# Performance work log

Hardware: AMD Instinct MI355X
Metric: run time of the kernel (lower is better)

## Reference

```python
import jax, jax.numpy as jnp
import numpy as np

EPS = 1e-6

def _exp_map0(v):
    # v: [..., D] tangent at origin with v[...,0]==0
    sp = v[..., 1:]
    n = jnp.sqrt(jnp.clip(jnp.sum(sp * sp, -1, keepdims=True), EPS))
    return jnp.concatenate([jnp.cosh(n), jnp.sinh(n) / n * sp], -1)

def _log_map0(x):
    x0 = x[..., :1]
    sp = x[..., 1:]
    n = jnp.sqrt(jnp.clip(jnp.sum(sp * sp, -1, keepdims=True), EPS))
    d = jnp.arccosh(jnp.clip(x0, 1.0 + EPS))
    return jnp.concatenate([jnp.zeros_like(x0), d / n * sp], -1)

def _pt_to_origin(x, v):
    # parallel transport v from T_x to T_o, o=(1,0,...,0):
    # PT(v) = v + <o,v>_L / (1 - <x,o>_L) * (x + o);  <o,v>_L=-v0, <x,o>_L=-x0
    coef = -v[..., :1] / (1.0 + x[..., :1])
    x_plus_o = jnp.concatenate([x[..., :1] + 1.0, x[..., 1:]], -1)
    return v + coef * x_plus_o

def _linear(h, W, b):
    # torch nn.Linear: h @ W.T + b, W: [out, in]
    return jnp.einsum('bne,de->bnd', h, W) + b

def setup_inputs() -> dict:
    key = jax.random.key(0)
    ks = jax.random.split(key, 8)
    B, N, d = 8, 2048, 256
    # manifold points via exp_map0 of small tangents
    t = jax.random.normal(ks[0], (B, N, d), jnp.float32) * 0.1
    x = _exp_map0(jnp.pad(t, ((0, 0), (0, 0), (1, 0))))
    # tangent velocity at x: project random u onto T_x (add <x,u>_L * x since <x,x>_L=-1)
    u = jax.random.normal(ks[1], (B, N, d + 1), jnp.float32) * 0.1
    xu = jnp.sum(x * u, -1, keepdims=True) - 2.0 * x[..., :1] * u[..., :1]  # Lorentz inner
    x_vel = u + xu * x
    s = 1.0 / np.sqrt(d)
    Wq = jax.random.normal(ks[2], (d, d), jnp.float32) * s
    Wk = jax.random.normal(ks[3], (d, d), jnp.float32) * s
    Wv = jax.random.normal(ks[4], (d, d), jnp.float32) * s
    bq = jnp.zeros((d,), jnp.float32)
    bk = jnp.zeros((d,), jnp.float32)
    bv = jnp.zeros((d,), jnp.float32)
    tau = jnp.ones((1,), jnp.float32)
    return {"x": x, "x_vel": x_vel, "Wq": Wq, "bq": bq, "Wk": Wk, "bk": bk,
            "Wv": Wv, "bv": bv, "tau": tau}

def reference(x, x_vel, Wq, bq, Wk, bk, Wv, bv, tau):
    lambda_penalty = 1.0
    log_x = _log_map0(x)
    x_tan = log_x[..., 1:]                                   # [B,N,d]
    q_s = _linear(x_tan, Wq, bq)
    k_s = _linear(x_tan, Wk, bk)
    v_s = _linear(x_tan, Wv, bv)
    pad = lambda h: jnp.pad(h, ((0, 0), (0, 0), (1, 0)))
    q = _exp_map0(pad(q_s))                                  # [B,N,D]
    k = _exp_map0(pad(k_s))
    log_v = pad(v_s)
    vel0 = _pt_to_origin(x, x_vel)
    q_vel = _linear(vel0[..., 1:], Wq, bq)                   # [B,N,d]
    k_vel = _linear(vel0[..., 1:], Wk, bk)
    # pairwise Lorentz distance: <q,k>_L = sum(q*k) - 2*q0*k0
    inner = jnp.einsum('bnd,bmd->bnm', q, k) \
            - 2.0 * q[..., 0][:, :, None] * k[..., 0][:, None, :]
    d_L = jnp.arccosh(jnp.clip(-inner, 1.0 + EPS))           # [B,N,N]
    q_sq = jnp.sum(q_vel * q_vel, -1)                        # [B,N]
    k_sq = jnp.sum(k_vel * k_vel, -1)
    qk = jnp.einsum('bnd,bmd->bnm', q_vel, k_vel)
    pen = jnp.clip(q_sq[:, :, None] + k_sq[:, None, :] - 2.0 * qk, 0.0)
    tau_c = jnp.clip(tau, 0.001)[0]
    logits = -(1.0 / tau_c) * d_L ** 2 - lambda_penalty * pen
    attn = jax.nn.softmax(logits, axis=-1)                   # [B,N,N]
    agg = jnp.einsum('bnm,bmd->bnd', attn, log_v)
    z = _exp_map0(agg)
    return z, attn, x_tan
```

## Files before the change

kernel.cpp:

```cpp
#include <hip/hip_runtime.h>
#include <math.h>

#define BB 8
#define NN 2048
#define DD 256
#define TT (BB*NN)
#define DP1 257
#define EPSF 1e-6f

typedef _Float16 f16;
typedef __attribute__((ext_vector_type(8))) _Float16 f16x8;
typedef __attribute__((ext_vector_type(4))) float f32x4;

#define BAR() asm volatile("s_barrier" ::: "memory")
#define WAIT_VM(N) asm volatile("s_waitcnt vmcnt(" #N ")" ::: "memory")
#define WAIT_LGKM0() asm volatile("s_waitcnt lgkmcnt(0)" ::: "memory")

__device__ __forceinline__ f32x4 mfma16(f16x8 a, f16x8 b, f32x4 c) {
  return __builtin_amdgcn_mfma_f32_16x16x32_f16(a, b, c, 0, 0, 0);
}
__device__ __forceinline__ void gll16(const f16* g, f16* l) {
  __builtin_amdgcn_global_load_lds(
      (const __attribute__((address_space(1))) void*)g,
      (__attribute__((address_space(3))) void*)l, 16, 0, 0);
}

__device__ __forceinline__ float wave_sum(float v) {
#pragma unroll
  for (int m = 1; m < 64; m <<= 1) v += __shfl_xor(v, m);
  return v;
}

__global__ __launch_bounds__(256) void prep_kernel(
    const float* __restrict__ x, const float* __restrict__ xv,
    float* __restrict__ xtan, f16* __restrict__ xtan_h, f16* __restrict__ vel0_h) {
  const int w = threadIdx.x >> 6, l = threadIdx.x & 63;
  const int tok = blockIdx.x * 4 + w;
  const float* xr = x  + (size_t)tok * DP1;
  const float* vr = xv + (size_t)tok * DP1;
  float x0 = xr[0];
  float sp[4];
  float ss = 0.f;
#pragma unroll
  for (int j = 0; j < 4; j++) { sp[j] = xr[1 + l + 64 * j]; ss = fmaf(sp[j], sp[j], ss); }
  ss = wave_sum(ss);
  float n  = sqrtf(fmaxf(ss, EPSF));
  float dd = acoshf(fmaxf(x0, 1.f + EPSF));
  float scl = dd / n;
  float coef = -vr[0] / (1.f + x0);
  const size_t base = (size_t)tok * DD;
#pragma unroll
  for (int j = 0; j < 4; j++) {
    float xt = scl * sp[j];
    xtan[base + l + 64 * j] = xt;
    xtan_h[base + l + 64 * j] = (f16)xt;
    vel0_h[base + l + 64 * j] = (f16)(vr[1 + l + 64 * j] + coef * sp[j]);
  }
}

__global__ __launch_bounds__(256) void wcast_kernel(
    const float* __restrict__ Wq, const float* __restrict__ Wk,
    const float* __restrict__ Wv, f16* __restrict__ Wh) {
  const int m = blockIdx.y;
  const int i = blockIdx.x * 256 + threadIdx.x;
  const float* W = (m == 0) ? Wq : ((m == 1) ? Wk : Wv);
  Wh[(size_t)m * DD * DD + i] = (f16)W[i];
}

__global__ __launch_bounds__(256, 2) void gemm_mfma(
    const f16* __restrict__ xtan_h, const f16* __restrict__ vel0_h,
    const f16* __restrict__ Wh,
    f16* __restrict__ qh, f16* __restrict__ kh, f16* __restrict__ vT,
    f16* __restrict__ qvh, f16* __restrict__ kvh,
    const float* __restrict__ bq, const float* __restrict__ bk,
    const float* __restrict__ bv) {
  __shared__ __align__(16) f16 sA[2 * 4096];
  __shared__ __align__(16) f16 sB[2 * 4096];
  const int tid = threadIdx.x;
  const int bm = blockIdx.x * 128;
  const int bn = blockIdx.y * 128;
  const int seg = bn >> 8;
  const int w = tid >> 6, l = tid & 63;
  const int wr = w >> 1, wc = w & 1;
  f32x4 acc[4][4] = {};
  const f16* Ab = ((seg < 3) ? xtan_h : vel0_h) + (size_t)bm * DD;
  const f16* Bb = Wh + (size_t)((seg < 3) ? bn : (bn - 768)) * DD;

  auto stage = [&](int nx) {
    const int half = nx & 1, k0 = nx * 32;
#pragma unroll
    for (int p = 0; p < 2; p++) {
      int u = tid + p * 256;
      int row = u >> 2;
      int q = (u & 3) ^ ((u >> 3) & 3);
      size_t go = (size_t)row * DD + k0 + q * 8;
      size_t lb = (size_t)half * 4096 + (size_t)(w * 64 + p * 256) * 8;
      gll16(Ab + go, sA + lb);
      gll16(Bb + go, sB + lb);
    }
  };

  stage(0);
  const int fq = ((l >> 4) ^ ((l >> 1) & 3)) * 8;
  for (int kt = 0; kt < 8; ++kt) {
    if (kt < 7) { stage(kt + 1); WAIT_VM(4); }
    else        { WAIT_VM(0); }
    BAR();
    const int co = (kt & 1) * 4096;
    f16x8 af[4], bf[4];
#pragma unroll
    for (int i = 0; i < 4; i++)
      af[i] = *(const f16x8*)(sA + co + (wr * 64 + i * 16 + (l & 15)) * 32 + fq);
#pragma unroll
    for (int j = 0; j < 4; j++)
      bf[j] = *(const f16x8*)(sB + co + (wc * 64 + j * 16 + (l & 15)) * 32 + fq);
#pragma unroll
    for (int i = 0; i < 4; i++)
#pragma unroll
      for (int j = 0; j < 4; j++)
        acc[i][j] = mfma16(af[i], bf[j], acc[i][j]);
    BAR();
  }

  f16* optr = (seg == 0) ? qh : (seg == 1) ? kh : (seg == 2) ? vT : (seg == 3) ? qvh : kvh;
  const float* bias = (seg == 0 || seg == 3) ? bq : (seg == 1 || seg == 4) ? bk : bv;
  const int ot = (seg == 2) ? 1 : 0;
  const int rl = (l >> 4) * 4, cl = l & 15;
#pragma unroll
  for (int i = 0; i < 4; i++) {
#pragma unroll
    for (int j = 0; j < 4; j++) {
      const int col = (bn & 255) + wc * 64 + j * 16 + cl;
      const float bvv = bias[col];
      const int row0 = bm + wr * 64 + i * 16 + rl;
      if (ot == 0) {
#pragma unroll
        for (int r = 0; r < 4; r++)
          optr[(size_t)(row0 + r) * DD + col] = (f16)(acc[i][j][r] + bvv);
      } else {
        __align__(8) f16 tmp[4];
#pragma unroll
        for (int r = 0; r < 4; r++) tmp[r] = (f16)(acc[i][j][r] + bvv);
        f16* dst = optr + ((size_t)((row0 >> 11) * DD + col)) * NN + (row0 & (NN - 1));
        *(uint2*)dst = *(const uint2*)tmp;
      }
    }
  }
}

__global__ __launch_bounds__(256) void scale_kernel(
    f16* __restrict__ qh, f16* __restrict__ kh,
    const f16* __restrict__ qvh, const f16* __restrict__ kvh,
    float* __restrict__ q0, float* __restrict__ k0v,
    float* __restrict__ q_sq, float* __restrict__ k_sq) {
  const int w = threadIdx.x >> 6, l = threadIdx.x & 63;
  const int tok = blockIdx.x * 4 + w;
  const size_t base = (size_t)tok * DD;
  float q[4], k[4];
  float sq = 0.f, sk = 0.f, svq = 0.f, svk = 0.f;
#pragma unroll
  for (int j = 0; j < 4; j++) {
    size_t off = base + l + 64 * j;
    q[j] = (float)qh[off];
    k[j] = (float)kh[off];
    float qv = (float)qvh[off], kv = (float)kvh[off];
    sq = fmaf(q[j], q[j], sq);
    sk = fmaf(k[j], k[j], sk);
    svq = fmaf(qv, qv, svq);
    svk = fmaf(kv, kv, svk);
  }
  sq = wave_sum(sq); sk = wave_sum(sk);
  svq = wave_sum(svq); svk = wave_sum(svk);
  float nq = sqrtf(fmaxf(sq, EPSF));
  float nk = sqrtf(fmaxf(sk, EPSF));
  float scq = sinhf(nq) / nq, sck = sinhf(nk) / nk;
#pragma unroll
  for (int j = 0; j < 4; j++) {
    size_t off = base + l + 64 * j;
    qh[off] = (f16)(q[j] * scq);
    kh[off] = (f16)(k[j] * sck);
  }
  if (l == 0) {
    q0[tok] = coshf(nq);
    k0v[tok] = coshf(nk);
    q_sq[tok] = svq;
    k_sq[tok] = svk;
  }
}

__global__ __launch_bounds__(256, 2) void logits_mfma(
    const f16* __restrict__ qh, const f16* __restrict__ kh,
    const f16* __restrict__ qvh, const f16* __restrict__ kvh,
    const float* __restrict__ q0a, const float* __restrict__ k0a,
    const float* __restrict__ qsqa, const float* __restrict__ ksqa,
    const float* __restrict__ tau, float* __restrict__ attn,
    float* __restrict__ psum) {
  __shared__ __align__(16) f16 sQ[2*4096], sK[2*4096], sQv[2*4096], sKv[2*4096];
  const int tid = threadIdx.x;
  const int bid = blockIdx.x;
  const int b = bid & 7;
  const int bq = ((bid >> 3) & 15) * 128;
  const int kti = bid >> 7;
  const int bk = kti * 128;
  const size_t tb = (size_t)b * NN;
  const f16* Q  = qh  + (tb + bq) * DD;
  const f16* Kp = kh  + (tb + bk) * DD;
  const f16* Qv = qvh + (tb + bq) * DD;
  const f16* Kv = kvh + (tb + bk) * DD;
  const int w = tid >> 6, l = tid & 63;
  const int wr = w >> 1, wc = w & 1;
  f32x4 accq[4][4] = {}, accv[4][4] = {};

  auto stage = [&](int nx) {
    const int half = nx & 1, k0 = nx * 32;
#pragma unroll
    for (int p = 0; p < 2; p++) {
      int u = tid + p * 256;
      int row = u >> 2;
      int q = (u & 3) ^ ((u >> 3) & 3);
      size_t go = (size_t)row * DD + k0 + q * 8;
      size_t lb = (size_t)half * 4096 + (size_t)(w * 64 + p * 256) * 8;
      gll16(Kp + go, sK  + lb);
      gll16(Q  + go, sQ  + lb);
      gll16(Kv + go, sKv + lb);
      gll16(Qv + go, sQv + lb);
    }
  };

  stage(0);
  const int fq = ((l >> 4) ^ ((l >> 1) & 3)) * 8;
  for (int kt = 0; kt < 8; ++kt) {
    if (kt < 7) { stage(kt + 1); WAIT_VM(8); }
    else        { WAIT_VM(0); }
    BAR();
    const int co = (kt & 1) * 4096;
    {
      f16x8 ak[4], bqf[4];
#pragma unroll
      for (int i = 0; i < 4; i++)
        ak[i] = *(const f16x8*)(sK + co + (wr * 64 + i * 16 + (l & 15)) * 32 + fq);
#pragma unroll
      for (int j = 0; j < 4; j++)
        bqf[j] = *(const f16x8*)(sQ + co + (wc * 64 + j * 16 + (l & 15)) * 32 + fq);
#pragma unroll
      for (int i = 0; i < 4; i++)
#pragma unroll
        for (int j = 0; j < 4; j++)
          accq[i][j] = mfma16(ak[i], bqf[j], accq[i][j]);
    }
    {
      f16x8 ak[4], bqf[4];
#pragma unroll
      for (int i = 0; i < 4; i++)
        ak[i] = *(const f16x8*)(sKv + co + (wr * 64 + i * 16 + (l & 15)) * 32 + fq);
#pragma unroll
      for (int j = 0; j < 4; j++)
        bqf[j] = *(const f16x8*)(sQv + co + (wc * 64 + j * 16 + (l & 15)) * 32 + fq);
#pragma unroll
      for (int i = 0; i < 4; i++)
#pragma unroll
        for (int j = 0; j < 4; j++)
          accv[i][j] = mfma16(ak[i], bqf[j], accv[i][j]);
    }
    BAR();
  }

  const int rl = (l >> 4) * 4, cl = l & 15;
  const float invt = 1.f / fmaxf(tau[0], 1e-3f);
  const float cc = invt * 0.4804530139182014f;
  float q0r[4], qsr[4];
  float4 k0c[4], ksc[4];
#pragma unroll
  for (int j = 0; j < 4; j++) {
    const int qq = bq + wc * 64 + j * 16 + cl;
    q0r[j] = q0a[tb + qq];
    qsr[j] = qsqa[tb + qq];
  }
#pragma unroll
  for (int i = 0; i < 4; i++) {
    const int kk = bk + wr * 64 + i * 16 + rl;
    k0c[i] = *(const float4*)(k0a + tb + kk);
    ksc[i] = *(const float4*)(ksqa + tb + kk);
  }
  const size_t obase = (size_t)b * NN * NN;
#pragma unroll
  for (int j = 0; j < 4; j++) {
    const int qq = bq + wc * 64 + j * 16 + cl;
    const float q0 = q0r[j], qs = qsr[j];
    float es = 0.f;
#pragma unroll
    for (int i = 0; i < 4; i++) {
      const int kk = bk + wr * 64 + i * 16 + rl;
      const float* k0p = (const float*)&k0c[i];
      const float* ksp = (const float*)&ksc[i];
      float4 o;
      float* op = (float*)&o;
#pragma unroll
      for (int r = 0; r < 4; r++) {
        float xv = fmaxf(fmaf(q0, k0p[r], -accq[i][j][r]), 1.f + EPSF);
        float s = sqrtf(fmaf(xv, xv, -1.f));
        float lg = __log2f(xv + s);
        float pen = fmaxf(fmaf(-2.f, accv[i][j][r], qs + ksp[r]), 0.f);
        float lo = fmaf(-cc * lg, lg, -pen);
        float ex = __expf(lo);
        op[r] = ex;
        es += ex;
      }
      *(float4*)(attn + obase + (size_t)qq * NN + kk) = o;
    }
    es += __shfl_xor(es, 16);
    es += __shfl_xor(es, 32);
    if ((l >> 4) == 0)
      psum[((size_t)(b * 16 + kti) * 2 + wr) * NN + qq] = es;
  }
}

__global__ __launch_bounds__(256, 2) void pv_fused(
    const float* __restrict__ psum, const f16* __restrict__ vT,
    float* __restrict__ attn, float* __restrict__ z) {
  __shared__ __align__(16) f16 sP[2][32 * 32];
  __shared__ __align__(16) f16 sV[3][256 * 32];
  __shared__ float invs_l[32];
  __shared__ float zsum[4][32];
  __shared__ float zsc[32];
  const int tid = threadIdx.x;
  const int bid = blockIdx.x;
  const int b = bid & 7;
  const int row0 = (bid >> 3) * 32;
  const int w = tid >> 6, l = tid & 63;
  float* slab = attn + ((size_t)b * NN + row0) * NN;
  const f16* Vb = vT + (size_t)b * DD * NN;

  if (tid < 32) {
    float s = 0.f;
#pragma unroll 4
    for (int p = 0; p < 32; p++) s += psum[((size_t)b * 32 + p) * NN + row0 + tid];
    invs_l[tid] = 1.f / s;
  }
  __syncthreads();
  const int prow = tid >> 3, pm4 = tid & 7;
  const float myinv = invs_l[prow];
  const int fq = ((l >> 4) ^ ((l >> 1) & 3)) * 8;
  const int spo = prow * 32 + ((pm4 >> 1) ^ ((prow >> 1) & 3)) * 8 + (pm4 & 1) * 4;
  f32x4 acc[2][4] = {};
  float4 pA, pB;

#define STAGEV(nx, vb) do { const int m0_ = (nx) * 32;                          \
    _Pragma("unroll")                                                           \
    for (int p_ = 0; p_ < 4; p_++) {                                            \
      int u_ = tid + p_ * 256;                                                  \
      int d_ = u_ >> 2;                                                         \
      int q_ = (u_ & 3) ^ ((u_ >> 3) & 3);                                      \
      gll16(Vb + (size_t)d_ * NN + m0_ + q_ * 8,                                \
            (f16*)&sV[vb][0] + (size_t)(w * 64 + p_ * 256) * 8);                \
    } } while (0)
#define LOADP(nx, reg) do {                                                     \
    reg = *(const float4*)(slab + (size_t)prow * NN + (nx) * 32 + pm4 * 4);     \
  } while (0)
#define USEP(nx, reg) do {                                                      \
    float e0_ = reg.x * myinv, e1_ = reg.y * myinv;                             \
    float e2_ = reg.z * myinv, e3_ = reg.w * myinv;                             \
    float4 ov_ = {e0_, e1_, e2_, e3_};                                          \
    *(float4*)(slab + (size_t)prow * NN + (nx) * 32 + pm4 * 4) = ov_;           \
    __align__(8) f16 tmp_[4] = {(f16)e0_, (f16)e1_, (f16)e2_, (f16)e3_};        \
    *(uint2*)(&sP[(nx) & 1][spo]) = *(const uint2*)tmp_;                        \
  } while (0)
#define COMPUTE(t, vb) do {                                                     \
    f16x8 af_[2], bf_[4];                                                       \
    _Pragma("unroll")                                                           \
    for (int i_ = 0; i_ < 2; i_++)                                              \
      af_[i_] = *(const f16x8*)(&sP[(t) & 1][(i_ * 16 + (l & 15)) * 32 + fq]);  \
    _Pragma("unroll")                                                           \
    for (int j_ = 0; j_ < 4; j_++)                                              \
      bf_[j_] = *(const f16x8*)((const f16*)&sV[vb][0] +                        \
                                (w * 64 + j_ * 16 + (l & 15)) * 32 + fq);       \
    _Pragma("unroll")                                                           \
    for (int i_ = 0; i_ < 2; i_++)                                              \
      _Pragma("unroll")                                                         \
      for (int j_ = 0; j_ < 4; j_++)                                            \
        acc[i_][j_] = mfma16(af_[i_], bf_[j_], acc[i_][j_]);                    \
  } while (0)

  STAGEV(0, 0); LOADP(0, pA);
  STAGEV(1, 1); LOADP(1, pB);
  WAIT_VM(5);
  USEP(0, pA);
  WAIT_LGKM0();
  BAR();

  int vb0 = 0;
  for (int tt = 0; tt < 32; ++tt) {
    {
      const int t = 2 * tt;
      const int vb_t = vb0;
      const int vb_s = (vb0 + 2 > 2) ? vb0 - 1 : vb0 + 2;
      if (t < 62) { STAGEV(t + 2, vb_s); LOADP(t + 2, pA); WAIT_VM(5); }
      else        { WAIT_VM(1); }
      if (t < 63) USEP(t + 1, pB);
      COMPUTE(t, vb_t);
      WAIT_LGKM0();
      BAR();
    }
    {
      const int t = 2 * tt + 1;
      const int vb_t = (vb0 + 1 > 2) ? vb0 - 2 : vb0 + 1;
      const int vb_s = vb0;
      if (t < 62)      { STAGEV(t + 2, vb_s); LOADP(t + 2, pB); WAIT_VM(5); }
      else if (t == 62){ WAIT_VM(1); }
      else             { WAIT_VM(0); }
      if (t < 63) USEP(t + 1, pA);
      COMPUTE(t, vb_t);
      WAIT_LGKM0();
      BAR();
    }
    vb0 = (vb0 + 2 > 2) ? vb0 - 1 : vb0 + 2;
  }
#undef STAGEV
#undef LOADP
#undef USEP
#undef COMPUTE

  const int rl4 = (l >> 4) * 4, cl = l & 15;
  float s2[2][4];
#pragma unroll
  for (int i = 0; i < 2; i++)
#pragma unroll
    for (int r = 0; r < 4; r++) {
      float s = 0.f;
#pragma unroll
      for (int j = 0; j < 4; j++) s = fmaf(acc[i][j][r], acc[i][j][r], s);
#pragma unroll
      for (int m = 1; m < 16; m <<= 1) s += __shfl_xor(s, m);
      s2[i][r] = s;
    }
  if (cl == 0) {
#pragma unroll
    for (int i = 0; i < 2; i++)
#pragma unroll
      for (int r = 0; r < 4; r++)
        zsum[w][i * 16 + rl4 + r] = s2[i][r];
  }
  __syncthreads();
  if (tid < 32) {
    float n2 = zsum[0][tid] + zsum[1][tid] + zsum[2][tid] + zsum[3][tid];
    float nn = sqrtf(fmaxf(n2, EPSF));
    zsc[tid] = sinhf(nn) / nn;
    z[(size_t)(b * NN + row0 + tid) * DP1] = coshf(nn);
  }
  __syncthreads();
#pragma unroll
  for (int i = 0; i < 2; i++)
#pragma unroll
    for (int r = 0; r < 4; r++) {
      const int row = i * 16 + rl4 + r;
      const float sc = zsc[row];
      const size_t zb = (size_t)(b * NN + row0 + row) * DP1 + 1;
#pragma unroll
      for (int j = 0; j < 4; j++)
        z[zb + w * 64 + j * 16 + cl] = acc[i][j][r] * sc;
    }
}

extern "C" void kernel_launch(void* const* d_in, const int* in_sizes, int n_in,
                              void* d_out, int out_size, void* d_ws, size_t ws_size,
                              hipStream_t stream) {
  const float* x   = (const float*)d_in[0];
  const float* xv  = (const float*)d_in[1];
  const float* Wq  = (const float*)d_in[2];
  const float* bq  = (const float*)d_in[3];
  const float* Wk  = (const float*)d_in[4];
  const float* bk  = (const float*)d_in[5];
  const float* Wv  = (const float*)d_in[6];
  const float* bv  = (const float*)d_in[7];
  const float* tau = (const float*)d_in[8];
  float* out = (float*)d_out;
  char* ws = (char*)d_ws;

  const size_t TD2 = (size_t)TT * DD * 2;

  f16*   qh     = (f16*)(ws);
  f16*   kh     = (f16*)(ws + TD2);
  f16*   qvh    = (f16*)(ws + 2 * TD2);
  f16*   kvh    = (f16*)(ws + 3 * TD2);
  f16*   vT     = (f16*)(ws + 4 * TD2);
  f16*   xtan_h = (f16*)(ws + 5 * TD2);
  f16*   vel0_h = (f16*)(ws + 6 * TD2);
  f16*   Wh     = (f16*)(ws + 7 * TD2);
  float* psum   = (float*)(ws + 7 * TD2 + 3 * DD * DD * 2);
  float* q0     = psum + (size_t)BB * 32 * NN;
  float* k0v    = q0 + TT;
  float* q_sq   = q0 + 2 * TT;
  float* k_sq   = q0 + 3 * TT;

  float* z_out    = out;
  float* attn_out = out + (size_t)TT * DP1;
  float* xtan_out = attn_out + (size_t)BB * NN * NN;

  prep_kernel<<<TT / 4, 256, 0, stream>>>(x, xv, xtan_out, xtan_h, vel0_h);
  wcast_kernel<<<dim3(DD * DD / 256, 3), 256, 0, stream>>>(Wq, Wk, Wv, Wh);

  gemm_mfma<<<dim3(TT / 128, 10), 256, 0, stream>>>(
      xtan_h, vel0_h, Wh, qh, kh, vT, qvh, kvh, bq, bk, bv);

  scale_kernel<<<TT / 4, 256, 0, stream>>>(qh, kh, qvh, kvh, q0, k0v, q_sq, k_sq);

  logits_mfma<<<NN / 128 * NN / 128 * BB, 256, 0, stream>>>(
      qh, kh, qvh, kvh, q0, k0v, q_sq, k_sq, tau, attn_out, psum);

  pv_fused<<<NN / 32 * BB, 256, 0, stream>>>(psum, vT, attn_out, z_out);
}
```

Before: 205.6 us.

## Rewrite PV kernel to stream P and V into registers, split QK staging

The PV kernel no longer stages P and V through LDS. Each wave loads attention rows and V fragments directly from global memory into registers, double-buffered. It normalizes them into f16 MFMA operands and writes the normalized attention back from the f16 operands. This removes LDS traffic and the LDS waits from the loop. The cost is redundant global reads of P across waves and attention output rounded through f16. The logits kernel splits staging so the Q/K tiles and the velocity tiles are fetched and consumed in separate phases, and MFMA loops are wrapped in s_setprio.

```diff
diff --git a/kernel.cpp b/kernel.cpp
--- a/kernel.cpp
+++ b/kernel.cpp
@@ -14,7 +14,6 @@
 
 #define BAR() asm volatile("s_barrier" ::: "memory")
 #define WAIT_VM(N) asm volatile("s_waitcnt vmcnt(" #N ")" ::: "memory")
-#define WAIT_LGKM0() asm volatile("s_waitcnt lgkmcnt(0)" ::: "memory")
 
 __device__ __forceinline__ f32x4 mfma16(f16x8 a, f16x8 b, f32x4 c) {
   return __builtin_amdgcn_mfma_f32_16x16x32_f16(a, b, c, 0, 0, 0);
@@ -29,6 +28,20 @@
 #pragma unroll
   for (int m = 1; m < 64; m <<= 1) v += __shfl_xor(v, m);
   return v;
+}
+
+__device__ __forceinline__ f16x8 nrm8(float4 a, float4 b, float s) {
+  f16x8 r;
+  r[0] = (f16)(a.x * s); r[1] = (f16)(a.y * s); r[2] = (f16)(a.z * s); r[3] = (f16)(a.w * s);
+  r[4] = (f16)(b.x * s); r[5] = (f16)(b.y * s); r[6] = (f16)(b.z * s); r[7] = (f16)(b.w * s);
+  return r;
+}
+
+__device__ __forceinline__ void st8(float* p, f16x8 v) {
+  float4 o0 = {(float)v[0], (float)v[1], (float)v[2], (float)v[3]};
+  float4 o1 = {(float)v[4], (float)v[5], (float)v[6], (float)v[7]};
+  *(float4*)p = o0;
+  *(float4*)(p + 4) = o1;
 }
 
 __global__ __launch_bounds__(256) void prep_kernel(
@@ -114,11 +127,13 @@
 #pragma unroll
     for (int j = 0; j < 4; j++)
       bf[j] = *(const f16x8*)(sB + co + (wc * 64 + j * 16 + (l & 15)) * 32 + fq);
+    __builtin_amdgcn_s_setprio(1);
 #pragma unroll
     for (int i = 0; i < 4; i++)
 #pragma unroll
       for (int j = 0; j < 4; j++)
         acc[i][j] = mfma16(af[i], bf[j], acc[i][j]);
+    __builtin_amdgcn_s_setprio(0);
     BAR();
   }
 
@@ -211,7 +226,7 @@
   const int wr = w >> 1, wc = w & 1;
   f32x4 accq[4][4] = {}, accv[4][4] = {};
 
-  auto stage = [&](int nx) {
+  auto stageKQ = [&](int nx) {
     const int half = nx & 1, k0 = nx * 32;
 #pragma unroll
     for (int p = 0; p < 2; p++) {
@@ -220,47 +235,67 @@
       int q = (u & 3) ^ ((u >> 3) & 3);
       size_t go = (size_t)row * DD + k0 + q * 8;
       size_t lb = (size_t)half * 4096 + (size_t)(w * 64 + p * 256) * 8;
-      gll16(Kp + go, sK  + lb);
-      gll16(Q  + go, sQ  + lb);
+      gll16(Kp + go, sK + lb);
+      gll16(Q  + go, sQ + lb);
+    }
+  };
+  auto stageVv = [&](int nx) {
+    const int half = nx & 1, k0 = nx * 32;
+#pragma unroll
+    for (int p = 0; p < 2; p++) {
+      int u = tid + p * 256;
+      int row = u >> 2;
+      int q = (u & 3) ^ ((u >> 3) & 3);
+      size_t go = (size_t)row * DD + k0 + q * 8;
+      size_t lb = (size_t)half * 4096 + (size_t)(w * 64 + p * 256) * 8;
       gll16(Kv + go, sKv + lb);
       gll16(Qv + go, sQv + lb);
     }
   };
 
-  stage(0);
+  stageKQ(0);
+  stageVv(0);
   const int fq = ((l >> 4) ^ ((l >> 1) & 3)) * 8;
   for (int kt = 0; kt < 8; ++kt) {
-    if (kt < 7) { stage(kt + 1); WAIT_VM(8); }
+    const int co = (kt & 1) * 4096;
+    if (kt < 7) { stageKQ(kt + 1); WAIT_VM(8); }
+    else        { WAIT_VM(4); }
+    BAR();
+    {
+      f16x8 ak[4], bqf[4];
+#pragma unroll
+      for (int i = 0; i < 4; i++)
+        ak[i] = *(const f16x8*)(sK + co + (wr * 64 + i * 16 + (l & 15)) * 32 + fq);
+#pragma unroll
+      for (int j = 0; j < 4; j++)
+        bqf[j] = *(const f16x8*)(sQ + co + (wc * 64 + j * 16 + (l & 15)) * 32 + fq);
+      __builtin_amdgcn_s_setprio(1);
+#pragma unroll
+      for (int i = 0; i < 4; i++)
+#pragma unroll
+        for (int j = 0; j < 4; j++)
+          accq[i][j] = mfma16(ak[i], bqf[j], accq[i][j]);
+      __builtin_amdgcn_s_setprio(0);
+    }
+    BAR();
+    if (kt < 7) { stageVv(kt + 1); WAIT_VM(8); }
     else        { WAIT_VM(0); }
     BAR();
-    const int co = (kt & 1) * 4096;
     {
       f16x8 ak[4], bqf[4];
 #pragma unroll
       for (int i = 0; i < 4; i++)
-        ak[i] = *(const f16x8*)(sK + co + (wr * 64 + i * 16 + (l & 15)) * 32 + fq);
-#pragma unroll
-      for (int j = 0; j < 4; j++)
-        bqf[j] = *(const f16x8*)(sQ + co + (wc * 64 + j * 16 + (l & 15)) * 32 + fq);
-#pragma unroll
-      for (int i = 0; i < 4; i++)
-#pragma unroll
-        for (int j = 0; j < 4; j++)
-          accq[i][j] = mfma16(ak[i], bqf[j], accq[i][j]);
-    }
-    {
-      f16x8 ak[4], bqf[4];
-#pragma unroll
-      for (int i = 0; i < 4; i++)
         ak[i] = *(const f16x8*)(sKv + co + (wr * 64 + i * 16 + (l & 15)) * 32 + fq);
 #pragma unroll
       for (int j = 0; j < 4; j++)
         bqf[j] = *(const f16x8*)(sQv + co + (wc * 64 + j * 16 + (l & 15)) * 32 + fq);
+      __builtin_amdgcn_s_setprio(1);
 #pragma unroll
       for (int i = 0; i < 4; i++)
 #pragma unroll
         for (int j = 0; j < 4; j++)
           accv[i][j] = mfma16(ak[i], bqf[j], accv[i][j]);
+      __builtin_amdgcn_s_setprio(0);
     }
     BAR();
   }
@@ -318,8 +353,6 @@
 __global__ __launch_bounds__(256, 2) void pv_fused(
     const float* __restrict__ psum, const f16* __restrict__ vT,
     float* __restrict__ attn, float* __restrict__ z) {
-  __shared__ __align__(16) f16 sP[2][32 * 32];
-  __shared__ __align__(16) f16 sV[3][256 * 32];
   __shared__ float invs_l[32];
   __shared__ float zsum[4][32];
   __shared__ float zsc[32];
@@ -328,8 +361,34 @@
   const int b = bid & 7;
   const int row0 = (bid >> 3) * 32;
   const int w = tid >> 6, l = tid & 63;
+  const int rlo = l & 15;
+  const int kq = l >> 4;
   float* slab = attn + ((size_t)b * NN + row0) * NN;
   const f16* Vb = vT + (size_t)b * DD * NN;
+
+  const float* pr0 = slab + (size_t)rlo * NN;
+  const float* pr1 = slab + (size_t)(16 + rlo) * NN;
+  const f16* vr[4];
+#pragma unroll
+  for (int j = 0; j < 4; j++) vr[j] = Vb + (size_t)(w * 64 + j * 16 + rlo) * NN;
+
+  float4 psrc0[4], psrc1[4];
+  f16x8 vreg0[4], vreg1[4];
+  f16x8 pst0 = {}, pst1 = {};
+  f32x4 acc[2][4] = {};
+
+#pragma unroll
+  for (int g = 0; g < 2; g++) {
+    const int mo = g * 32 + kq * 8;
+    float4* ps = g ? psrc1 : psrc0;
+    f16x8* vs = g ? vreg1 : vreg0;
+    ps[0] = *(const float4*)(pr0 + mo);
+    ps[1] = *(const float4*)(pr0 + mo + 4);
+    ps[2] = *(const float4*)(pr1 + mo);
+    ps[3] = *(const float4*)(pr1 + mo + 4);
+#pragma unroll
+    for (int j = 0; j < 4; j++) vs[j] = *(const f16x8*)(vr[j] + mo);
+  }
 
   if (tid < 32) {
     float s = 0.f;
@@ -338,89 +397,62 @@
     invs_l[tid] = 1.f / s;
   }
   __syncthreads();
-  const int prow = tid >> 3, pm4 = tid & 7;
-  const float myinv = invs_l[prow];
-  const int fq = ((l >> 4) ^ ((l >> 1) & 3)) * 8;
-  const int spo = prow * 32 + ((pm4 >> 1) ^ ((prow >> 1) & 3)) * 8 + (pm4 & 1) * 4;
-  f32x4 acc[2][4] = {};
-  float4 pA, pB;
-
-#define STAGEV(nx, vb) do { const int m0_ = (nx) * 32;                          \
-    _Pragma("unroll")                                                           \
-    for (int p_ = 0; p_ < 4; p_++) {                                            \
-      int u_ = tid + p_ * 256;                                                  \
-      int d_ = u_ >> 2;                                                         \
-      int q_ = (u_ & 3) ^ ((u_ >> 3) & 3);                                      \
-      gll16(Vb + (size_t)d_ * NN + m0_ + q_ * 8,                                \
-            (f16*)&sV[vb][0] + (size_t)(w * 64 + p_ * 256) * 8);                \
-    } } while (0)
-#define LOADP(nx, reg) do {                                                     \
-    reg = *(const float4*)(slab + (size_t)prow * NN + (nx) * 32 + pm4 * 4);     \
-  } while (0)
-#define USEP(nx, reg) do {                                                      \
-    float e0_ = reg.x * myinv, e1_ = reg.y * myinv;                             \
-    float e2_ = reg.z * myinv, e3_ = reg.w * myinv;                             \
-    float4 ov_ = {e0_, e1_, e2_, e3_};                                          \
-    *(float4*)(slab + (size_t)prow * NN + (nx) * 32 + pm4 * 4) = ov_;           \
-    __align__(8) f16 tmp_[4] = {(f16)e0_, (f16)e1_, (f16)e2_, (f16)e3_};        \
-    *(uint2*)(&sP[(nx) & 1][spo]) = *(const uint2*)tmp_;                        \
-  } while (0)
-#define COMPUTE(t, vb) do {                                                     \
-    f16x8 af_[2], bf_[4];                                                       \
-    _Pragma("unroll")                                                           \
-    for (int i_ = 0; i_ < 2; i_++)                                              \
-      af_[i_] = *(const f16x8*)(&sP[(t) & 1][(i_ * 16 + (l & 15)) * 32 + fq]);  \
-    _Pragma("unroll")                                                           \
-    for (int j_ = 0; j_ < 4; j_++)                                              \
-      bf_[j_] = *(const f16x8*)((const f16*)&sV[vb][0] +                        \
-                                (w * 64 + j_ * 16 + (l & 15)) * 32 + fq);       \
-    _Pragma("unroll")                                                           \
-    for (int i_ = 0; i_ < 2; i_++)                                              \
-      _Pragma("unroll")                                                         \
-      for (int j_ = 0; j_ < 4; j_++)                                            \
-        acc[i_][j_] = mfma16(af_[i_], bf_[j_], acc[i_][j_]);                    \
-  } while (0)
-
-  STAGEV(0, 0); LOADP(0, pA);
-  STAGEV(1, 1); LOADP(1, pB);
-  WAIT_VM(5);
-  USEP(0, pA);
-  WAIT_LGKM0();
-  BAR();
-
-  int vb0 = 0;
+  const float inv0 = invs_l[rlo];
+  const float inv1 = invs_l[16 + rlo];
+
+  const int i_st = w >> 1;
+  const bool st_act = ((rlo >> 3) == (w & 1));
+  float* stbase = slab + (size_t)(i_st * 16 + rlo) * NN + kq * 8;
+
   for (int tt = 0; tt < 32; ++tt) {
     {
-      const int t = 2 * tt;
-      const int vb_t = vb0;
-      const int vb_s = (vb0 + 2 > 2) ? vb0 - 1 : vb0 + 2;
-      if (t < 62) { STAGEV(t + 2, vb_s); LOADP(t + 2, pA); WAIT_VM(5); }
-      else        { WAIT_VM(1); }
-      if (t < 63) USEP(t + 1, pB);
-      COMPUTE(t, vb_t);
-      WAIT_LGKM0();
+      WAIT_VM(8);
+      f16x8 a0 = nrm8(psrc0[0], psrc0[1], inv0);
+      f16x8 a1 = nrm8(psrc0[2], psrc0[3], inv1);
+#pragma unroll
+      for (int j = 0; j < 4; j++) {
+        acc[0][j] = mfma16(a0, vreg0[j], acc[0][j]);
+        acc[1][j] = mfma16(a1, vreg0[j], acc[1][j]);
+      }
+      if (tt > 0 && st_act) st8(stbase + (2 * tt - 1) * 32, pst1);
+      pst0 = (i_st == 0) ? a0 : a1;
+      if (tt < 31) {
+        const int mo = (2 * tt + 2) * 32 + kq * 8;
+        psrc0[0] = *(const float4*)(pr0 + mo);
+        psrc0[1] = *(const float4*)(pr0 + mo + 4);
+        psrc0[2] = *(const float4*)(pr1 + mo);
+        psrc0[3] = *(const float4*)(pr1 + mo + 4);
+#pragma unroll
+        for (int j = 0; j < 4; j++) vreg0[j] = *(const f16x8*)(vr[j] + mo);
+      }
       BAR();
     }
     {
-      const int t = 2 * tt + 1;
-      const int vb_t = (vb0 + 1 > 2) ? vb0 - 2 : vb0 + 1;
-      const int vb_s = vb0;
-      if (t < 62)      { STAGEV(t + 2, vb_s); LOADP(t + 2, pB); WAIT_VM(5); }
-      else if (t == 62){ WAIT_VM(1); }
-      else             { WAIT_VM(0); }
-      if (t < 63) USEP(t + 1, pA);
-      COMPUTE(t, vb_t);
-      WAIT_LGKM0();
+      if (tt < 31) { WAIT_VM(8); } else { WAIT_VM(0); }
+      f16x8 a0 = nrm8(psrc1[0], psrc1[1], inv0);
+      f16x8 a1 = nrm8(psrc1[2], psrc1[3], inv1);
+#pragma unroll
+      for (int j = 0; j < 4; j++) {
+        acc[0][j] = mfma16(a0, vreg1[j], acc[0][j]);
+        acc[1][j] = mfma16(a1, vreg1[j], acc[1][j]);
+      }
+      if (st_act) st8(stbase + (2 * tt) * 32, pst0);
+      pst1 = (i_st == 0) ? a0 : a1;
+      if (tt < 31) {
+        const int mo = (2 * tt + 3) * 32 + kq * 8;
+        psrc1[0] = *(const float4*)(pr0 + mo);
+        psrc1[1] = *(const float4*)(pr0 + mo + 4);
+        psrc1[2] = *(const float4*)(pr1 + mo);
+        psrc1[3] = *(const float4*)(pr1 + mo + 4);
+#pragma unroll
+        for (int j = 0; j < 4; j++) vreg1[j] = *(const f16x8*)(vr[j] + mo);
+      }
       BAR();
     }
-    vb0 = (vb0 + 2 > 2) ? vb0 - 1 : vb0 + 2;
-  }
-#undef STAGEV
-#undef LOADP
-#undef USEP
-#undef COMPUTE
-
-  const int rl4 = (l >> 4) * 4, cl = l & 15;
+  }
+  if (st_act) st8(stbase + 63 * 32, pst1);
+
+  const int rl4 = kq * 4, cl = rlo;
   float s2[2][4];
 #pragma unroll
   for (int i = 0; i < 2; i++)
```

Result: slower. 268.1 us (+30.4%).

## Split logits GEMM into sequential Q/K and velocity passes with halved LDS

Applied to the files above, without the earlier changes.

The logits kernel previously staged four operand tiles (Q, K, Qv, Kv) per k-step into 32 KB of double-buffered LDS. It now runs two back-to-back 8-step loops, first the distance GEMM and then the velocity GEMM, each staging only two tiles into 16 KB of shared memory. The first tile of the second pass is prefetched at the end of the first. This halves LDS use, which may allow more resident blocks, but doubles the number of barriers and loop iterations. s_setprio raises wave priority around the MFMA blocks in both the projection and logits kernels.

```diff
diff --git a/kernel.cpp b/kernel.cpp
--- a/kernel.cpp
+++ b/kernel.cpp
@@ -114,11 +114,13 @@
 #pragma unroll
     for (int j = 0; j < 4; j++)
       bf[j] = *(const f16x8*)(sB + co + (wc * 64 + j * 16 + (l & 15)) * 32 + fq);
+    __builtin_amdgcn_s_setprio(1);
 #pragma unroll
     for (int i = 0; i < 4; i++)
 #pragma unroll
       for (int j = 0; j < 4; j++)
         acc[i][j] = mfma16(af[i], bf[j], acc[i][j]);
+    __builtin_amdgcn_s_setprio(0);
     BAR();
   }
 
@@ -195,7 +197,8 @@
     const float* __restrict__ qsqa, const float* __restrict__ ksqa,
     const float* __restrict__ tau, float* __restrict__ attn,
     float* __restrict__ psum) {
-  __shared__ __align__(16) f16 sQ[2*4096], sK[2*4096], sQv[2*4096], sKv[2*4096];
+  __shared__ __align__(16) f16 sA[2 * 4096];
+  __shared__ __align__(16) f16 sB[2 * 4096];
   const int tid = threadIdx.x;
   const int bid = blockIdx.x;
   const int b = bid & 7;
@@ -210,8 +213,9 @@
   const int w = tid >> 6, l = tid & 63;
   const int wr = w >> 1, wc = w & 1;
   f32x4 accq[4][4] = {}, accv[4][4] = {};
-
-  auto stage = [&](int nx) {
+  const int fq = ((l >> 4) ^ ((l >> 1) & 3)) * 8;
+
+  auto stage2 = [&](const f16* Ksrc, const f16* Qsrc, int nx) {
     const int half = nx & 1, k0 = nx * 32;
 #pragma unroll
     for (int p = 0; p < 2; p++) {
@@ -220,50 +224,48 @@
       int q = (u & 3) ^ ((u >> 3) & 3);
       size_t go = (size_t)row * DD + k0 + q * 8;
       size_t lb = (size_t)half * 4096 + (size_t)(w * 64 + p * 256) * 8;
-      gll16(Kp + go, sK  + lb);
-      gll16(Q  + go, sQ  + lb);
-      gll16(Kv + go, sKv + lb);
-      gll16(Qv + go, sQv + lb);
+      gll16(Ksrc + go, sA + lb);
+      gll16(Qsrc + go, sB + lb);
     }
   };
 
-  stage(0);
-  const int fq = ((l >> 4) ^ ((l >> 1) & 3)) * 8;
+#define LMFMA(ACC)                                                              \
+  {                                                                             \
+    f16x8 ak[4], bqf[4];                                                        \
+    _Pragma("unroll")                                                           \
+    for (int i = 0; i < 4; i++)                                                 \
+      ak[i] = *(const f16x8*)(sA + co + (wr * 64 + i * 16 + (l & 15)) * 32 + fq); \
+    _Pragma("unroll")                                                           \
+    for (int j = 0; j < 4; j++)                                                 \
+      bqf[j] = *(const f16x8*)(sB + co + (wc * 64 + j * 16 + (l & 15)) * 32 + fq); \
+    __builtin_amdgcn_s_setprio(1);                                              \
+    _Pragma("unroll")                                                           \
+    for (int i = 0; i < 4; i++)                                                 \
+      _Pragma("unroll")                                                         \
+      for (int j = 0; j < 4; j++)                                               \
+        ACC[i][j] = mfma16(ak[i], bqf[j], ACC[i][j]);                           \
+    __builtin_amdgcn_s_setprio(0);                                              \
+  }
+
+  stage2(Kp, Q, 0);
   for (int kt = 0; kt < 8; ++kt) {
-    if (kt < 7) { stage(kt + 1); WAIT_VM(8); }
+    if (kt < 7) stage2(Kp, Q, kt + 1);
+    else        stage2(Kv, Qv, 0);
+    WAIT_VM(4);
+    BAR();
+    const int co = (kt & 1) * 4096;
+    LMFMA(accq)
+    BAR();
+  }
+  for (int kt = 0; kt < 8; ++kt) {
+    if (kt < 7) { stage2(Kv, Qv, kt + 1); WAIT_VM(4); }
     else        { WAIT_VM(0); }
     BAR();
     const int co = (kt & 1) * 4096;
-    {
-      f16x8 ak[4], bqf[4];
-#pragma unroll
-      for (int i = 0; i < 4; i++)
-        ak[i] = *(const f16x8*)(sK + co + (wr * 64 + i * 16 + (l & 15)) * 32 + fq);
-#pragma unroll
-      for (int j = 0; j < 4; j++)
-        bqf[j] = *(const f16x8*)(sQ + co + (wc * 64 + j * 16 + (l & 15)) * 32 + fq);
-#pragma unroll
-      for (int i = 0; i < 4; i++)
-#pragma unroll
-        for (int j = 0; j < 4; j++)
-          accq[i][j] = mfma16(ak[i], bqf[j], accq[i][j]);
-    }
-    {
-      f16x8 ak[4], bqf[4];
-#pragma unroll
-      for (int i = 0; i < 4; i++)
-        ak[i] = *(const f16x8*)(sKv + co + (wr * 64 + i * 16 + (l & 15)) * 32 + fq);
-#pragma unroll
-      for (int j = 0; j < 4; j++)
-        bqf[j] = *(const f16x8*)(sQv + co + (wc * 64 + j * 16 + (l & 15)) * 32 + fq);
-#pragma unroll
-      for (int i = 0; i < 4; i++)
-#pragma unroll
-        for (int j = 0; j < 4; j++)
-          accv[i][j] = mfma16(ak[i], bqf[j], accv[i][j]);
-    }
+    LMFMA(accv)
     BAR();
   }
+#undef LMFMA
 
   const int rl = (l >> 4) * 4, cl = l & 15;
   const float invt = 1.f / fmaxf(tau[0], 1e-3f);
```

Measured after the change: 193.8 us. 5.7% less time.
